# Kernel optimization log

Hardware: AMD Instinct MI355X
Metric: run time of the kernel (lower is better)

The kernel has to match this reference:

```python
import jax, jax.numpy as jnp
import numpy as np
from jax import lax

IOU_THRESHOLD = 0.2  # hardcoded in TinyModel.forward
N = 8192


def setup_inputs() -> dict:
    key = jax.random.key(0)
    k1, k2, k3 = jax.random.split(key, 3)
    # Build valid boxes: top-left corner in [0, 1000), size in [1, 51)
    xy = jax.random.uniform(k1, (N, 2), dtype=jnp.float32) * 1000.0
    wh = jax.random.uniform(k2, (N, 2), dtype=jnp.float32) * 50.0 + 1.0
    rois = jnp.concatenate([xy, xy + wh], axis=-1)  # [N,4] = (x1,y1,x2,y2)
    scores = jax.random.uniform(k3, (N,), dtype=jnp.float32)
    return {"rois": rois, "scores": scores}


def _pairwise_iou(boxes):
    # boxes: [N,4]; returns [N,N] IoU (torchvision convention, no +1)
    x1, y1, x2, y2 = boxes[:, 0], boxes[:, 1], boxes[:, 2], boxes[:, 3]
    area = (x2 - x1) * (y2 - y1)                       # [N]
    ix1 = jnp.maximum(x1[:, None], x1[None, :])
    iy1 = jnp.maximum(y1[:, None], y1[None, :])
    ix2 = jnp.minimum(x2[:, None], x2[None, :])
    iy2 = jnp.minimum(y2[:, None], y2[None, :])
    iw = jnp.clip(ix2 - ix1, 0.0)
    ih = jnp.clip(iy2 - iy1, 0.0)
    inter = iw * ih                                    # [N,N]
    union = area[:, None] + area[None, :] - inter
    return inter / jnp.maximum(union, 1e-9)


def _nms_keep_mask(rois, scores, thr):
    n = rois.shape[0]
    order = jnp.argsort(-scores)                       # descending by score
    boxes = rois[order]                                # [N,4] sorted
    over = _pairwise_iou(boxes) > thr                  # [N,N] bool
    idx = jnp.arange(n)
    # box i may only suppress lower-scored boxes j > i (strict upper triangle)
    over = over & (idx[None, :] > idx[:, None])

    def body(i, keep):
        row = over[i] & keep[i]                        # suppress only if i survives
        return keep & ~row

    keep_sorted = lax.fori_loop(0, n, body, jnp.ones((n,), dtype=bool))
    # scatter back to original box ordering
    keep = jnp.zeros((n,), dtype=bool).at[order].set(keep_sorted)
    return keep


def reference(rois, scores):
    # NMS returns a data-dependent set of kept indices in torch; for fixed
    # shapes we return the scores with suppressed boxes zeroed (original order).
    keep = _nms_keep_mask(rois, scores, IOU_THRESHOLD)  # [N] bool
    return jnp.where(keep, scores, 0.0)
```

## Files before the change

### kernel.cpp

```cpp
#include <hip/hip_runtime.h>

#define N 8192
#define CAP 64
#define THR 0.2f


__global__ __launch_bounds__(256) void rank_scatter_kernel(const float* __restrict__ rois,
                                                           const float* __restrict__ scores,
                                                           unsigned* __restrict__ order,
                                                           unsigned* __restrict__ cellCnt,
                                                           unsigned* __restrict__ cellS,
                                                           float4* __restrict__ cellBox) {
    __shared__ float sc[1024];
    const int t = threadIdx.x, b = blockIdx.x;

    const int il = t >> 3, sub = t & 7;
    const int i = b * 32 + il;
    const float si = scores[i];
    unsigned c = 0;
    for (int tile = 0; tile < 8; ++tile) {
        ((float4*)sc)[t] = ((const float4*)scores)[tile * 256 + t];
        __syncthreads();
        #pragma unroll 16
        for (int q = 0; q < 128; ++q) {
            int jj = q * 8 + sub;
            float sj = sc[jj];
            int j = tile * 1024 + jj;
            c += (sj > si) || (sj == si && j < i);
        }
        __syncthreads();
    }
    c += __shfl_xor(c, 1);
    c += __shfl_xor(c, 2);
    c += __shfl_xor(c, 4);
    if (sub == 0) {
        order[c] = (unsigned)i;
        float4 bx = ((const float4*)rois)[i];
        int cx = (int)(bx.x * 0.015625f); if (cx > 15) cx = 15;
        int cy = (int)(bx.y * 0.015625f); if (cy > 15) cy = 15;
        int cell = cy * 16 + cx;
        unsigned slot = atomicAdd(&cellCnt[cell], 1u);
        if (slot < 96u) {
            cellS[cell * 96 + slot] = c;
            cellBox[cell * 96 + slot] = bx;
        }
    }
}

__device__ __forceinline__ bool iou_over(const float4 A, const float4 B) {
    float areaA = __fmul_rn(__fsub_rn(A.z, A.x), __fsub_rn(A.w, A.y));
    float areaB = __fmul_rn(__fsub_rn(B.z, B.x), __fsub_rn(B.w, B.y));
    float ix1 = fmaxf(A.x, B.x);
    float iy1 = fmaxf(A.y, B.y);
    float ix2 = fminf(A.z, B.z);
    float iy2 = fminf(A.w, B.w);
    float iw = fmaxf(__fsub_rn(ix2, ix1), 0.0f);
    float ih = fmaxf(__fsub_rn(iy2, iy1), 0.0f);
    float inter = __fmul_rn(iw, ih);
    float uni = __fsub_rn(__fadd_rn(areaA, areaB), inter);
    float iou = __fdiv_rn(inter, fmaxf(uni, 1e-9f));
    return iou > THR;
}

__global__ __launch_bounds__(256) void edge2_kernel(const float4* __restrict__ cellBox,
                                                    const unsigned* __restrict__ cellS,
                                                    const unsigned* __restrict__ cellCnt,
                                                    unsigned long long* __restrict__ premask,
                                                    unsigned* __restrict__ cnt,
                                                    unsigned short* __restrict__ edgesTS,
                                                    unsigned short* __restrict__ edgesOvf) {
    const int c = blockIdx.x;
    const int cx = c & 15, cy = c >> 4;
    __shared__ float4 ob[96];
    __shared__ unsigned os[96];
    const int t = threadIdx.x;
    int on = (int)cellCnt[c];
    if (on > 96) on = 96;
    if (t < on) { ob[t] = cellBox[c * 96 + t]; os[t] = cellS[c * 96 + t]; }
    __syncthreads();
    if (on == 0) return;

    const int offs[5][2] = {{0,0},{1,0},{-1,1},{0,1},{1,1}};
    #pragma unroll
    for (int q = 0; q < 5; ++q) {
        const int nx = cx + offs[q][0], ny = cy + offs[q][1];
        if (nx < 0 || nx > 15 || ny > 15) continue;
        const int d = ny * 16 + nx;
        int dn = (int)cellCnt[d];
        if (dn > 96) dn = 96;
        const int npairs = on * dn;
        for (int p = t; p < npairs; p += 256) {
            const int i = p / dn, j = p - i * dn;
            if (q == 0 && j <= i) continue;
            const float4 B = cellBox[d * 96 + j];
            const unsigned sb = cellS[d * 96 + j];
            if (iou_over(ob[i], B)) {
                const unsigned sa = os[i];
                const unsigned is = sa < sb ? sa : sb;
                const unsigned js = sa < sb ? sb : sa;
                if ((is >> 6) == (js >> 6)) {
                    atomicOr(&premask[js], 1ull << (is & 63));
                } else {
                    unsigned pos = atomicAdd(&cnt[is], 1u);
                    if (pos < 8) {
                        edgesTS[(((is >> 6) * 2 + (pos >> 2)) * 64 + (is & 63)) * 4 + (pos & 3)] =
                            (unsigned short)js;
                    } else if (pos < CAP) {
                        edgesOvf[(size_t)is * 56 + (pos - 8)] = (unsigned short)js;
                    }
                }
            }
        }
    }
}

#define PF(B, CH) do { \
    int ch_ = (CH); \
    if (ch_ < 128) { \
        int pb_ = ch_ * 64 + lane; \
        pm##B = premask[pb_]; \
        n##B  = cnt[pb_]; \
        ea##B = edgesT[(ch_ * 2 + 0) * 64 + lane]; \
        eb##B = edgesT[(ch_ * 2 + 1) * 64 + lane]; \
    } \
} while (0)

#define APPLY(i, W, SH) { \
    unsigned d_ = (unsigned)((W) >> (SH)) & 0xFFFFu; \
    bool v_ = (i) < nn_; \
    unsigned a_ = v_ ? (d_ >> 5) : (unsigned)lane; \
    unsigned m_ = v_ ? ~(1u << (d_ & 31)) : ~0u; \
    atomicAnd(&alive[a_], m_); }

#define STEP(B, C) do { \
    const unsigned av_ = (alive[(C) * 2 + (lane >> 5)] >> (lane & 31)) & 1u; \
    unsigned long long anz = __ballot(pm##B != 0ull); \
    unsigned long long kept = __ballot(av_ != 0u); \
    if (anz != 0ull) { \
        bool mydec = !av_ || (pm##B == 0ull); \
        unsigned long long decided = __ballot(mydec); \
        kept = __ballot(av_ && (pm##B == 0ull)); \
        while (decided != ~0ull) { \
            bool ready = !mydec && ((pm##B & ~decided) == 0ull); \
            bool k_ = ready && ((pm##B & kept) == 0ull); \
            kept |= __ballot(k_); \
            decided |= __ballot(ready); \
            mydec = mydec || ready; \
        } \
    } \
    if (lane == 0) keptw[(C)] = kept; \
    const unsigned kb_ = (unsigned)(kept >> lane) & 1u; \
    unsigned nn_ = kb_ ? (n##B > 8u ? 8u : n##B) : 0u; \
    APPLY(0u, ea##B, 0)  APPLY(1u, ea##B, 16) APPLY(2u, ea##B, 32) APPLY(3u, ea##B, 48) \
    APPLY(4u, eb##B, 0)  APPLY(5u, eb##B, 16) APPLY(6u, eb##B, 32) APPLY(7u, eb##B, 48) \
    if (__any(kb_ && n##B > 8u)) { \
        unsigned nf_ = kb_ ? (n##B > CAP ? (unsigned)CAP : n##B) : 0u; \
        for (unsigned e_ = 8; e_ < nf_; ++e_) { \
            unsigned d_ = edgesOvf[(size_t)((C) * 64 + lane) * 56 + (e_ - 8)]; \
            atomicAnd(&alive[d_ >> 5], ~(1u << (d_ & 31))); \
        } \
    } \
    PF(B, (C) + 8); \
    asm volatile("s_waitcnt lgkmcnt(0)" ::: "memory"); \
} while (0)

__global__ __launch_bounds__(64, 1)
void resolve_kernel(const unsigned long long* __restrict__ premask,
                    const unsigned* __restrict__ cnt,
                    const unsigned long long* __restrict__ edgesT,
                    const unsigned short* __restrict__ edgesOvf,
                    unsigned long long* __restrict__ keptw) {
    __shared__ unsigned alive[256];
    const int lane = threadIdx.x;
    #pragma unroll
    for (int w = 0; w < 4; ++w) alive[w * 64 + lane] = 0xFFFFFFFFu;
    asm volatile("s_waitcnt lgkmcnt(0)" ::: "memory");

    unsigned long long pm0, pm1, pm2, pm3, pm4, pm5, pm6, pm7;
    unsigned n0, n1, n2, n3, n4, n5, n6, n7;
    unsigned long long ea0, ea1, ea2, ea3, ea4, ea5, ea6, ea7;
    unsigned long long eb0, eb1, eb2, eb3, eb4, eb5, eb6, eb7;

    PF(0, 0); PF(1, 1); PF(2, 2); PF(3, 3);
    PF(4, 4); PF(5, 5); PF(6, 6); PF(7, 7);

    for (int cc = 0; cc < 128; cc += 8) {
        STEP(0, cc + 0); STEP(1, cc + 1); STEP(2, cc + 2); STEP(3, cc + 3);
        STEP(4, cc + 4); STEP(5, cc + 5); STEP(6, cc + 6); STEP(7, cc + 7);
    }
}

__global__ __launch_bounds__(256) void out_kernel(const float* __restrict__ scores,
                                                  const unsigned* __restrict__ order,
                                                  const unsigned long long* __restrict__ keptw,
                                                  float* __restrict__ out) {
    const int s = blockIdx.x * 256 + threadIdx.x;
    const unsigned orig = order[s];
    const unsigned keep = (unsigned)((keptw[s >> 6] >> (s & 63)) & 1ull);
    out[orig] = keep ? scores[orig] : 0.0f;
}

extern "C" void kernel_launch(void* const* d_in, const int* in_sizes, int n_in,
                              void* d_out, int out_size, void* d_ws, size_t ws_size,
                              hipStream_t stream) {
    const float* rois   = (const float*)d_in[0];
    const float* scores = (const float*)d_in[1];
    float* out = (float*)d_out;

    char* ws = (char*)d_ws;
    unsigned*            cnt      = (unsigned*)(ws);
    unsigned long long*  premask  = (unsigned long long*)(ws + 32768);
    unsigned*            cellCnt  = (unsigned*)(ws + 98304);
    unsigned*            order    = (unsigned*)(ws + 102400);
    unsigned*            cellS    = (unsigned*)(ws + 135168);
    float4*              cellBox  = (float4*)(ws + 262144);
    unsigned long long*  edgesT   = (unsigned long long*)(ws + 655360);
    unsigned short*      edgesOvf = (unsigned short*)(ws + 786432);
    unsigned long long*  keptw    = (unsigned long long*)(ws + 1703936);

    hipMemsetAsync(ws, 0, 99328, stream);

    rank_scatter_kernel<<<256, 256, 0, stream>>>(rois, scores, order,
                                                 cellCnt, cellS, cellBox);
    edge2_kernel<<<256, 256, 0, stream>>>(cellBox, cellS, cellCnt, premask, cnt,
                                          (unsigned short*)edgesT, edgesOvf);
    resolve_kernel<<<1, 64, 0, stream>>>(premask, cnt, edgesT, edgesOvf, keptw);
    out_kernel<<<32, 256, 0, stream>>>(scores, order, keptw, out);
}
```

Before: 135.8 us.

## Widen per-row inline edge slots to 32 and skip overflow path via flag

Raises the number of cross-chunk suppression edges stored inline per box from 8 to 32, laid out transposed so the serial resolve wave loads them coalesced into registers. The overflow list shrinks to 32 entries. A global flag set by the edge kernel lets the resolve kernel pick a template variant with no overflow loop when nothing spilled. Prefetch depth drops from 8 to 4 chunks to pay for the larger register footprint. The intent is to avoid slow per-lane global overflow reads in the serial loop, at the cost of more prefetch traffic and register pressure.

```diff
diff --git a/kernel.cpp b/kernel.cpp
--- a/kernel.cpp
+++ b/kernel.cpp
@@ -68,7 +68,8 @@
                                                     unsigned long long* __restrict__ premask,
                                                     unsigned* __restrict__ cnt,
                                                     unsigned short* __restrict__ edgesTS,
-                                                    unsigned short* __restrict__ edgesOvf) {
+                                                    unsigned short* __restrict__ edgesOvf,
+                                                    unsigned* __restrict__ ovfFlag) {
     const int c = blockIdx.x;
     const int cx = c & 15, cy = c >> 4;
     __shared__ float4 ob[96];
@@ -102,11 +103,12 @@
                     atomicOr(&premask[js], 1ull << (is & 63));
                 } else {
                     unsigned pos = atomicAdd(&cnt[is], 1u);
-                    if (pos < 8) {
-                        edgesTS[(((is >> 6) * 2 + (pos >> 2)) * 64 + (is & 63)) * 4 + (pos & 3)] =
+                    if (pos < 32) {
+                        edgesTS[(((is >> 6) * 8 + (pos >> 2)) * 64 + (is & 63)) * 4 + (pos & 3)] =
                             (unsigned short)js;
                     } else if (pos < CAP) {
-                        edgesOvf[(size_t)is * 56 + (pos - 8)] = (unsigned short)js;
+                        edgesOvf[(size_t)is * 32 + (pos - 32)] = (unsigned short)js;
+                        atomicOr(ovfFlag, 1u);
                     }
                 }
             }
@@ -114,14 +116,16 @@
     }
 }
 
-#define PF(B, CH) do { \
+
+#define PF4(B, CH) do { \
     int ch_ = (CH); \
     if (ch_ < 128) { \
         int pb_ = ch_ * 64 + lane; \
         pm##B = premask[pb_]; \
         n##B  = cnt[pb_]; \
-        ea##B = edgesT[(ch_ * 2 + 0) * 64 + lane]; \
-        eb##B = edgesT[(ch_ * 2 + 1) * 64 + lane]; \
+        const unsigned long long* er_ = edgesT + (size_t)ch_ * 512 + lane; \
+        e0##B = er_[0];   e1##B = er_[64];  e2##B = er_[128]; e3##B = er_[192]; \
+        e4##B = er_[256]; e5##B = er_[320]; e6##B = er_[384]; e7##B = er_[448]; \
     } \
 } while (0)
 
@@ -132,7 +136,7 @@
     unsigned m_ = v_ ? ~(1u << (d_ & 31)) : ~0u; \
     atomicAnd(&alive[a_], m_); }
 
-#define STEP(B, C) do { \
+#define STEP4(B, C) do { \
     const unsigned av_ = (alive[(C) * 2 + (lane >> 5)] >> (lane & 31)) & 1u; \
     unsigned long long anz = __ballot(pm##B != 0ull); \
     unsigned long long kept = __ballot(av_ != 0u); \
@@ -150,25 +154,58 @@
     } \
     if (lane == 0) keptw[(C)] = kept; \
     const unsigned kb_ = (unsigned)(kept >> lane) & 1u; \
-    unsigned nn_ = kb_ ? (n##B > 8u ? 8u : n##B) : 0u; \
-    APPLY(0u, ea##B, 0)  APPLY(1u, ea##B, 16) APPLY(2u, ea##B, 32) APPLY(3u, ea##B, 48) \
-    APPLY(4u, eb##B, 0)  APPLY(5u, eb##B, 16) APPLY(6u, eb##B, 32) APPLY(7u, eb##B, 48) \
-    if (__any(kb_ && n##B > 8u)) { \
-        unsigned nf_ = kb_ ? (n##B > CAP ? (unsigned)CAP : n##B) : 0u; \
-        for (unsigned e_ = 8; e_ < nf_; ++e_) { \
-            unsigned d_ = edgesOvf[(size_t)((C) * 64 + lane) * 56 + (e_ - 8)]; \
-            atomicAnd(&alive[d_ >> 5], ~(1u << (d_ & 31))); \
+    const unsigned deg_ = n##B; \
+    unsigned nn_ = kb_ ? (deg_ > 32u ? 32u : deg_) : 0u; \
+    APPLY(0u,  e0##B, 0) APPLY(1u,  e0##B, 16) APPLY(2u,  e0##B, 32) APPLY(3u,  e0##B, 48) \
+    APPLY(4u,  e1##B, 0) APPLY(5u,  e1##B, 16) APPLY(6u,  e1##B, 32) APPLY(7u,  e1##B, 48) \
+    if (__any(nn_ > 8u)) { \
+        APPLY(8u,  e2##B, 0) APPLY(9u,  e2##B, 16) APPLY(10u, e2##B, 32) APPLY(11u, e2##B, 48) \
+        APPLY(12u, e3##B, 0) APPLY(13u, e3##B, 16) APPLY(14u, e3##B, 32) APPLY(15u, e3##B, 48) \
+        APPLY(16u, e4##B, 0) APPLY(17u, e4##B, 16) APPLY(18u, e4##B, 32) APPLY(19u, e4##B, 48) \
+        APPLY(20u, e5##B, 0) APPLY(21u, e5##B, 16) APPLY(22u, e5##B, 32) APPLY(23u, e5##B, 48) \
+        APPLY(24u, e6##B, 0) APPLY(25u, e6##B, 16) APPLY(26u, e6##B, 32) APPLY(27u, e6##B, 48) \
+        APPLY(28u, e7##B, 0) APPLY(29u, e7##B, 16) APPLY(30u, e7##B, 32) APPLY(31u, e7##B, 48) \
+    } \
+    if constexpr (OVF) { \
+        if (__any(kb_ && deg_ > 32u)) { \
+            unsigned nf_ = kb_ ? (deg_ > (unsigned)CAP ? (unsigned)CAP : deg_) : 0u; \
+            for (unsigned e_ = 32; e_ < nf_; ++e_) { \
+                unsigned d_ = edgesOvf[(size_t)((C) * 64 + lane) * 32 + (e_ - 32)]; \
+                atomicAnd(&alive[d_ >> 5], ~(1u << (d_ & 31))); \
+            } \
         } \
     } \
-    PF(B, (C) + 8); \
+    PF4(B, (C) + 4); \
     asm volatile("s_waitcnt lgkmcnt(0)" ::: "memory"); \
 } while (0)
+
+template <bool OVF>
+__device__ __forceinline__ void resolve_body(const unsigned long long* __restrict__ premask,
+                                             const unsigned* __restrict__ cnt,
+                                             const unsigned long long* __restrict__ edgesT,
+                                             const unsigned short* __restrict__ edgesOvf,
+                                             unsigned long long* __restrict__ keptw,
+                                             unsigned* alive, const int lane) {
+    unsigned long long pm0, pm1, pm2, pm3;
+    unsigned n0, n1, n2, n3;
+    unsigned long long e00, e10, e20, e30, e40, e50, e60, e70;
+    unsigned long long e01, e11, e21, e31, e41, e51, e61, e71;
+    unsigned long long e02, e12, e22, e32, e42, e52, e62, e72;
+    unsigned long long e03, e13, e23, e33, e43, e53, e63, e73;
+
+    PF4(0, 0); PF4(1, 1); PF4(2, 2); PF4(3, 3);
+
+    for (int cc = 0; cc < 128; cc += 4) {
+        STEP4(0, cc + 0); STEP4(1, cc + 1); STEP4(2, cc + 2); STEP4(3, cc + 3);
+    }
+}
 
 __global__ __launch_bounds__(64, 1)
 void resolve_kernel(const unsigned long long* __restrict__ premask,
                     const unsigned* __restrict__ cnt,
                     const unsigned long long* __restrict__ edgesT,
                     const unsigned short* __restrict__ edgesOvf,
+                    const unsigned* __restrict__ ovfFlag,
                     unsigned long long* __restrict__ keptw) {
     __shared__ unsigned alive[256];
     const int lane = threadIdx.x;
@@ -176,17 +213,10 @@
     for (int w = 0; w < 4; ++w) alive[w * 64 + lane] = 0xFFFFFFFFu;
     asm volatile("s_waitcnt lgkmcnt(0)" ::: "memory");
 
-    unsigned long long pm0, pm1, pm2, pm3, pm4, pm5, pm6, pm7;
-    unsigned n0, n1, n2, n3, n4, n5, n6, n7;
-    unsigned long long ea0, ea1, ea2, ea3, ea4, ea5, ea6, ea7;
-    unsigned long long eb0, eb1, eb2, eb3, eb4, eb5, eb6, eb7;
-
-    PF(0, 0); PF(1, 1); PF(2, 2); PF(3, 3);
-    PF(4, 4); PF(5, 5); PF(6, 6); PF(7, 7);
-
-    for (int cc = 0; cc < 128; cc += 8) {
-        STEP(0, cc + 0); STEP(1, cc + 1); STEP(2, cc + 2); STEP(3, cc + 3);
-        STEP(4, cc + 4); STEP(5, cc + 5); STEP(6, cc + 6); STEP(7, cc + 7);
+    if (*ovfFlag == 0u) {
+        resolve_body<false>(premask, cnt, edgesT, edgesOvf, keptw, alive, lane);
+    } else {
+        resolve_body<true>(premask, cnt, edgesT, edgesOvf, keptw, alive, lane);
     }
 }
 
@@ -211,19 +241,20 @@
     unsigned*            cnt      = (unsigned*)(ws);
     unsigned long long*  premask  = (unsigned long long*)(ws + 32768);
     unsigned*            cellCnt  = (unsigned*)(ws + 98304);
+    unsigned*            ovfFlag  = (unsigned*)(ws + 99328);
     unsigned*            order    = (unsigned*)(ws + 102400);
     unsigned*            cellS    = (unsigned*)(ws + 135168);
     float4*              cellBox  = (float4*)(ws + 262144);
     unsigned long long*  edgesT   = (unsigned long long*)(ws + 655360);
-    unsigned short*      edgesOvf = (unsigned short*)(ws + 786432);
+    unsigned short*      edgesOvf = (unsigned short*)(ws + 1179648);
     unsigned long long*  keptw    = (unsigned long long*)(ws + 1703936);
 
-    hipMemsetAsync(ws, 0, 99328, stream);
+    hipMemsetAsync(ws, 0, 99840, stream);
 
     rank_scatter_kernel<<<256, 256, 0, stream>>>(rois, scores, order,
                                                  cellCnt, cellS, cellBox);
     edge2_kernel<<<256, 256, 0, stream>>>(cellBox, cellS, cellCnt, premask, cnt,
-                                          (unsigned short*)edgesT, edgesOvf);
-    resolve_kernel<<<1, 64, 0, stream>>>(premask, cnt, edgesT, edgesOvf, keptw);
+                                          (unsigned short*)edgesT, edgesOvf, ovfFlag);
+    resolve_kernel<<<1, 64, 0, stream>>>(premask, cnt, edgesT, edgesOvf, ovfFlag, keptw);
     out_kernel<<<32, 256, 0, stream>>>(scores, order, keptw, out);
 }
```

New measurement: 160.0 us. +17.8%, slower.
